# Kernel optimization log

Measured on AMD Instinct MI355X. Metric: run time of the kernel, lower is better.

Reference implementation:

```python
import jax, jax.numpy as jnp
import numpy as np
from jax import lax

DIM = 180
NUM_HEADS = 6
WS = 16                     # window_size
OWS = 24                    # overlap_win_size = int(16 * 1.5)
PAD = (OWS - WS) // 2       # 4
EPS = 1e-5


def setup_inputs() -> dict:
    key = jax.random.key(0)
    ks = jax.random.split(key, 4)
    B, H, W, C = 1, 256, 256, DIM
    x = jax.random.normal(ks[0], (B, H * W, C), dtype=jnp.float32)
    s = 0.05  # keep logits in a sane range
    return {
        "x": x,
        "norm_w": jnp.ones((C,), jnp.float32),
        "norm_b": jnp.zeros((C,), jnp.float32),
        "q_w": jax.random.normal(ks[1], (C, C), jnp.float32) * s,
        "q_b": jnp.zeros((C,), jnp.float32),
        "kv_w": jax.random.normal(ks[2], (C, 2 * C), jnp.float32) * s,
        "kv_b": jnp.zeros((2 * C,), jnp.float32),
        "proj_w": jax.random.normal(ks[3], (C, C), jnp.float32) * s,
        "proj_b": jnp.zeros((C,), jnp.float32),
        "H": H,
        "W": W,
    }


def _ocab(x, norm_w, norm_b, q_w, q_b, kv_w, kv_b, proj_w, proj_b, H, W):
    B, N, C = x.shape
    nh, hd = NUM_HEADS, C // NUM_HEADS
    scale = hd ** (-0.5)
    nHw, nWw = H // WS, W // WS
    nW = nHw * nWw

    shortcut = x
    # LayerNorm
    mu = jnp.mean(x, axis=-1, keepdims=True)
    var = jnp.var(x, axis=-1, keepdims=True)
    xn = (x - mu) * lax.rsqrt(var + EPS) * norm_w + norm_b

    feat = xn.reshape(B, H, W, C)

    # --- query: non-overlapping window partition -> [B*nW, WS*WS, C]
    qw = feat.reshape(B, nHw, WS, nWw, WS, C).transpose(0, 1, 3, 2, 4, 5)
    qw = qw.reshape(B * nW, WS * WS, C)
    q = qw @ q_w + q_b

    # --- key/value: overlapping windows via unfold (kernel=OWS, stride=WS, pad=PAD)
    feat_chw = feat.transpose(0, 3, 1, 2)  # [B, C, H, W]
    patches = lax.conv_general_dilated_patches(
        feat_chw, filter_shape=(OWS, OWS), window_strides=(WS, WS),
        padding=((PAD, PAD), (PAD, PAD)))  # [B, C*OWS*OWS, nHw, nWw], channel-major
    kv_feat = patches.reshape(B, C, OWS * OWS, nW).transpose(0, 3, 2, 1)
    kv_feat = kv_feat.reshape(B * nW, OWS * OWS, C)
    kv = kv_feat @ kv_w + kv_b
    k, v = jnp.split(kv, 2, axis=-1)

    # --- multi-head attention: 256 queries vs 576 keys per window
    q = q.reshape(B * nW, WS * WS, nh, hd).transpose(0, 2, 1, 3)
    k = k.reshape(B * nW, OWS * OWS, nh, hd).transpose(0, 2, 1, 3)
    v = v.reshape(B * nW, OWS * OWS, nh, hd).transpose(0, 2, 1, 3)

    attn = jnp.einsum('whqd,whkd->whqk', q, k) * scale
    attn = jax.nn.softmax(attn, axis=-1)
    out = jnp.einsum('whqk,whkd->whqd', attn, v)
    out = out.transpose(0, 2, 1, 3).reshape(B * nW, WS * WS, C)
    out = out @ proj_w + proj_b

    # --- window reverse + residual
    out = out.reshape(B, nHw, nWw, WS, WS, C).transpose(0, 1, 3, 2, 4, 5)
    out = out.reshape(B, N, C)
    return shortcut + out


def reference(x, norm_w, norm_b, q_w, q_b, kv_w, kv_b, proj_w, proj_b, H, W):
    return _ocab(x, norm_w, norm_b, q_w, q_b, kv_w, kv_b, proj_w, proj_b, H, W)
```

## Files before the change

kernel.cpp:

```cpp
#include <hip/hip_runtime.h>
#include <math.h>

typedef __bf16 bf16x8 __attribute__((ext_vector_type(8)));
typedef float f32x4 __attribute__((ext_vector_type(4)));
typedef unsigned short ushort_t;

static __device__ __forceinline__ unsigned short f2bf(float f) {
  union { float f; unsigned int u; } c; c.f = f;
  unsigned int u = c.u;
  unsigned int r = u + 0x7FFFu + ((u >> 16) & 1u);
  return (unsigned short)(r >> 16);
}

#define CDIM 180
#define CPAD 192
#define NTOK 65536

#define SCL2E 0.26339361f

static __device__ __forceinline__ unsigned pk_bf(float a, float b) {
  union { float f; unsigned u; } ca, cb; ca.f = a; cb.f = b;
  return __builtin_amdgcn_perm(cb.u, ca.u, 0x07060302u);
}

__global__ __launch_bounds__(256) void prep_k(
    const float* __restrict__ q_w, const float* __restrict__ q_b,
    const float* __restrict__ kv_w, const float* __restrict__ kv_b,
    const float* __restrict__ p_w, const float* __restrict__ p_b,
    ushort_t* __restrict__ wqkvt, ushort_t* __restrict__ pwt,
    float* __restrict__ qkvb, float* __restrict__ pbp,
    ushort_t* __restrict__ k_bias_row, ushort_t* __restrict__ vt4_bias_grp)
{
  int i = blockIdx.x * 256 + threadIdx.x;
  if (i < 110592) {
    int n = i / 192, k = i % 192;
    float v = 0.f;
    if (k < CDIM) {
      if (n < 192) { int h = n >> 5, d = n & 31; if (d < 30) v = q_w[k * CDIM + h * 30 + d] * SCL2E; }
      else { int cn = n - 192; int part = cn >= 192; int c2 = cn - part * 192;
             int h = c2 >> 5, d = c2 & 31;
             if (d < 30) v = kv_w[k * 360 + part * 180 + h * 30 + d]; }
    }
    wqkvt[i] = f2bf(v);
    return;
  }
  i -= 110592;
  if (i < 36864) {
    int n = i / 192, r = i % 192, h = r >> 5, d = r & 31;
    float v = (d < 30 && n < CDIM) ? p_w[(h * 30 + d) * CDIM + n] : 0.f;
    pwt[i] = f2bf(v);
    return;
  }
  i -= 36864;
  if (i < 576) {
    float v = 0.f;
    if (i < 192) { int h = i >> 5, d = i & 31; if (d < 30) v = q_b[h * 30 + d] * SCL2E; }
    else { int cn = i - 192; int part = cn >= 192; int c2 = cn - part * 192;
           int h = c2 >> 5, d = c2 & 31;
           if (d < 30) v = kv_b[part * 180 + h * 30 + d];
           else if (part == 1 && d == 30) v = 1.0f; }
    qkvb[i] = v;
    return;
  }
  i -= 576;
  if (i < 192) { pbp[i] = (i < CDIM) ? p_b[i] : 0.f; return; }
  i -= 192;
  if (i < 192) {
    int h = i >> 5, d = i & 31;
    k_bias_row[i] = (d < 30) ? f2bf(kv_b[h * 30 + d]) : (ushort_t)0;
    return;
  }
  i -= 192;
  if (i < 768) {
    int d = i >> 2, h = d >> 5, dd = d & 31;
    float v = 0.f;
    if (dd < 30) v = kv_b[180 + h * 30 + dd];
    else if (dd == 30) v = 1.0f;
    vt4_bias_grp[i] = f2bf(v);
    return;
  }
}

__global__ __launch_bounds__(256) void ln_k(const float* __restrict__ x,
    const float* __restrict__ nw, const float* __restrict__ nb,
    ushort_t* __restrict__ xn)
{
  const int lane = threadIdx.x & 63, wave = threadIdx.x >> 6;
  const int row = blockIdx.x * 4 + wave;
  const float* xr = x + (size_t)row * CDIM;
  float f0 = xr[lane];
  float f1 = xr[lane + 64];
  float f2 = (lane < 52) ? xr[lane + 128] : 0.f;
  float sum = f0 + f1 + f2;
  float sq = f0 * f0 + f1 * f1 + f2 * f2;
  #pragma unroll
  for (int off = 1; off < 64; off <<= 1) {
    sum += __shfl_xor(sum, off, 64);
    sq  += __shfl_xor(sq, off, 64);
  }
  const float inv_n = 1.0f / 180.0f;
  float mean = sum * inv_n;
  float var = sq * inv_n - mean * mean;
  float rs = rsqrtf(var + 1e-5f);
  ushort_t* xo = xn + (size_t)row * CPAD;
  #pragma unroll
  for (int e = 0; e < 3; ++e) {
    int col = lane + e * 64;
    float v = 0.f;
    if (col < CDIM) v = (( (e==0)?f0 : (e==1)?f1 : f2 ) - mean) * rs * nw[col] + nb[col];
    xo[col] = f2bf(v);
  }
}

template<int MODE>
__global__ __launch_bounds__(256) void gemm_k(const ushort_t* __restrict__ A,
    const ushort_t* __restrict__ Wt, const float* __restrict__ bias,
    ushort_t* __restrict__ q_out, ushort_t* __restrict__ k_out,
    ushort_t* __restrict__ vt_out,
    float* __restrict__ outf, const float* __restrict__ resid)
{
  constexpr int NT = (MODE == 0) ? 9 : 3;
  __shared__ __align__(16) ushort_t aS[128 * 200];
  const int tid = threadIdx.x;
  const int lane = tid & 63, wave = tid >> 6;
  const int quad = lane >> 4, l16 = lane & 15;
  const int wm = wave & 1, wn = wave >> 1;
  const int bm = blockIdx.x;

  {
    const ushort_t* Ab = A + (size_t)bm * 128 * 192;
    #pragma unroll
    for (int it = 0; it < 12; ++it) {
      int f = it * 256 + tid;
      int row = f / 24, kq = f % 24;
      uint4 v = *reinterpret_cast<const uint4*>(Ab + row * 192 + kq * 8);
      *reinterpret_cast<uint4*>(&aS[row * 200 + kq * 8]) = v;
    }
  }
  __syncthreads();

  for (int nt0 = 0; nt0 < NT; ++nt0) {
    f32x4 acc[4][2] = {};
    #pragma unroll
    for (int ks = 0; ks < 6; ++ks) {
      bf16x8 af[4], bfr[2];
      #pragma unroll
      for (int nt = 0; nt < 2; ++nt) {
        int n = nt0 * 64 + wn * 32 + nt * 16 + l16;
        bfr[nt] = *reinterpret_cast<const bf16x8*>(Wt + (size_t)n * 192 + ks * 32 + quad * 8);
      }
      #pragma unroll
      for (int mt = 0; mt < 4; ++mt)
        af[mt] = *reinterpret_cast<const bf16x8*>(&aS[(wm * 64 + mt * 16 + l16) * 200 + ks * 32 + quad * 8]);
      #pragma unroll
      for (int mt = 0; mt < 4; ++mt)
        #pragma unroll
        for (int nt = 0; nt < 2; ++nt)
          acc[mt][nt] = __builtin_amdgcn_mfma_f32_16x16x32_bf16(af[mt], bfr[nt], acc[mt][nt], 0, 0, 0);
    }
    #pragma unroll
    for (int mt = 0; mt < 4; ++mt) {
      int row = bm * 128 + wm * 64 + mt * 16 + quad * 4;
      #pragma unroll
      for (int nt = 0; nt < 2; ++nt) {
        int ncol = nt0 * 64 + wn * 32 + nt * 16 + l16;
        float bv = bias[ncol];
        if (MODE == 0 && nt0 >= 6) {
          int d = ncol - 384;
          unsigned p0 = pk_bf(acc[mt][nt][0] + bv, acc[mt][nt][1] + bv);
          unsigned p1 = pk_bf(acc[mt][nt][2] + bv, acc[mt][nt][3] + bv);
          uint2 val; val.x = p0; val.y = p1;
          *reinterpret_cast<uint2*>(vt_out + (size_t)row * 192 + d * 4) = val;
        } else {
          #pragma unroll
          for (int r = 0; r < 4; ++r) {
            int rr = row + r;
            float v = acc[mt][nt][r] + bv;
            if (MODE == 0) {
              if (ncol < 192) q_out[(size_t)rr * CPAD + ncol] = f2bf(v);
              else k_out[(size_t)rr * CPAD + (ncol - 192)] = f2bf(v);
            } else {
              if (ncol < CDIM) outf[(size_t)rr * CDIM + ncol] = v + resid[(size_t)rr * CDIM + ncol];
            }
          }
        }
      }
    }
  }
}

__global__ __launch_bounds__(256, 4) void attn_k(const ushort_t* __restrict__ q_tok,
    const ushort_t* __restrict__ k_tok, const ushort_t* __restrict__ vt4,
    ushort_t* __restrict__ ao)
{
  const int w = blockIdx.x, h = blockIdx.y;
  const int tid = threadIdx.x;
  const int lane = tid & 63, wave = tid >> 6;
  const int quad = lane >> 4, l16 = lane & 15;
  const int wy = w >> 4, wx = w & 15;
  const int tok0 = wy * 16 * 256 + wx * 16;
  const int hc = h * 32;
  const int ybase = wy * 16 - 4, xbase = wx * 16 - 4;

  bf16x8 qf[4];
  #pragma unroll
  for (int qt = 0; qt < 4; ++qt) {
    int qi = wave * 64 + qt * 16 + l16;
    int token = tok0 + (qi >> 4) * 256 + (qi & 15);
    qf[qt] = *reinterpret_cast<const bf16x8*>(q_tok + (size_t)token * CPAD + hc + quad * 8);
  }

  const int key0 = ((l16 >> 2) << 3) + (l16 & 3);

  int kpy[3][2], ktx[3][2]; bool kxin[3][2];
  int vpy[3][2], vtx[3][2]; bool vxin[3][2];
  #pragma unroll
  for (int cm = 0; cm < 3; ++cm) {
    #pragma unroll
    for (int j = 0; j < 2; ++j) {
      int pk = 32 * cm + key0 + 4 * j;
      int py = pk / 24, px = pk - py * 24;
      kpy[cm][j] = py; ktx[cm][j] = xbase + px;
      kxin[cm][j] = (unsigned)(xbase + px) < 256u;
      int pv = 32 * cm + quad * 8 + 4 * j;
      int pyv = pv / 24, pxv = pv - pyv * 24;
      vpy[cm][j] = pyv; vtx[cm][j] = xbase + pxv;
      vxin[cm][j] = (unsigned)(xbase + pxv) < 256u;
    }
  }
  const int dOff0 = (hc + l16) * 4, dOff1 = (hc + 16 + l16) * 4;

  f32x4 o[4][2] = {};
  f32x4 zero = {0.f, 0.f, 0.f, 0.f};

  #pragma unroll
  for (int c = 0; c < 18; ++c) {
    const int cm = c % 3, c3 = c / 3;
    const int yrow = ybase + 4 * c3;
    bf16x8 kf[2];
    #pragma unroll
    for (int kt = 0; kt < 2; ++kt) {
      int y = yrow + kpy[cm][kt];
      bool inb = kxin[cm][kt] && ((unsigned)y < 256u);
      int t = inb ? (y * 256 + ktx[cm][kt]) : NTOK;
      kf[kt] = *reinterpret_cast<const bf16x8*>(k_tok + (size_t)t * CPAD + hc + quad * 8);
    }
    unsigned vv[2][4];
    #pragma unroll
    for (int h2 = 0; h2 < 2; ++h2) {
      int y = yrow + vpy[cm][h2];
      bool inb = vxin[cm][h2] && ((unsigned)y < 256u);
      int t = inb ? (y * 256 + vtx[cm][h2]) : NTOK;
      const ushort_t* gp = vt4 + (size_t)t * 192;
      uint2 v0 = *reinterpret_cast<const uint2*>(gp + dOff0);
      uint2 v1 = *reinterpret_cast<const uint2*>(gp + dOff1);
      vv[0][h2 * 2] = v0.x; vv[0][h2 * 2 + 1] = v0.y;
      vv[1][h2 * 2] = v1.x; vv[1][h2 * 2 + 1] = v1.y;
    }
    bf16x8 vf[2];
    #pragma unroll
    for (int dt = 0; dt < 2; ++dt) {
      union { unsigned u[4]; bf16x8 v; } a_;
      a_.u[0] = vv[dt][0]; a_.u[1] = vv[dt][1];
      a_.u[2] = vv[dt][2]; a_.u[3] = vv[dt][3];
      vf[dt] = a_.v;
    }
    #pragma unroll
    for (int qt = 0; qt < 4; ++qt) {
      f32x4 s0 = __builtin_amdgcn_mfma_f32_16x16x32_bf16(kf[0], qf[qt], zero, 0, 0, 0);
      f32x4 s1 = __builtin_amdgcn_mfma_f32_16x16x32_bf16(kf[1], qf[qt], zero, 0, 0, 0);
      union { unsigned u[4]; bf16x8 v; } pk;
      pk.u[0] = pk_bf(__builtin_amdgcn_exp2f(s0[0]), __builtin_amdgcn_exp2f(s0[1]));
      pk.u[1] = pk_bf(__builtin_amdgcn_exp2f(s0[2]), __builtin_amdgcn_exp2f(s0[3]));
      pk.u[2] = pk_bf(__builtin_amdgcn_exp2f(s1[0]), __builtin_amdgcn_exp2f(s1[1]));
      pk.u[3] = pk_bf(__builtin_amdgcn_exp2f(s1[2]), __builtin_amdgcn_exp2f(s1[3]));
      #pragma unroll
      for (int dt = 0; dt < 2; ++dt)
        o[qt][dt] = __builtin_amdgcn_mfma_f32_16x16x32_bf16(pk.v, vf[dt], o[qt][dt], 0, 0, 0);
    }
  }

  #pragma unroll
  for (int qt = 0; qt < 4; ++qt) {
    #pragma unroll
    for (int r = 0; r < 4; ++r) {
      float l = __shfl(o[qt][1][r], (lane & 48) + 14, 64);
      float inv = 1.0f / l;
      int qi = wave * 64 + qt * 16 + quad * 4 + r;
      int token = tok0 + (qi >> 4) * 256 + (qi & 15);
      ao[(size_t)token * CPAD + hc + l16]      = f2bf(o[qt][0][r] * inv);
      ao[(size_t)token * CPAD + hc + 16 + l16] = f2bf(o[qt][1][r] * inv);
    }
  }
}

extern "C" void kernel_launch(void* const* d_in, const int* in_sizes, int n_in,
                              void* d_out, int out_size, void* d_ws, size_t ws_size,
                              hipStream_t stream) {
  const float* x      = (const float*)d_in[0];
  const float* norm_w = (const float*)d_in[1];
  const float* norm_b = (const float*)d_in[2];
  const float* q_w    = (const float*)d_in[3];
  const float* q_b    = (const float*)d_in[4];
  const float* kv_w   = (const float*)d_in[5];
  const float* kv_b   = (const float*)d_in[6];
  const float* p_w    = (const float*)d_in[7];
  const float* p_b    = (const float*)d_in[8];

  char* base = (char*)d_ws;
  size_t off = 0;
  auto alloc = [&](size_t bytes) { char* p = base + off; off = (off + bytes + 255) & ~(size_t)255; return p; };
  ushort_t* xn_p  = (ushort_t*)alloc((size_t)NTOK * CPAD * 2);
  ushort_t* q_tok = (ushort_t*)alloc((size_t)NTOK * CPAD * 2);
  ushort_t* k_tok = (ushort_t*)alloc((size_t)(NTOK + 1) * CPAD * 2);
  ushort_t* vt4   = (ushort_t*)alloc((size_t)(NTOK + 4) * 192 * 2);
  ushort_t* wqkvt = (ushort_t*)alloc(576 * 192 * 2);
  ushort_t* pwt   = (ushort_t*)alloc(192 * 192 * 2);
  float* qkvb = (float*)alloc(576 * 4);
  float* pbp  = (float*)alloc(192 * 4);
  ushort_t* ao = xn_p;

  prep_k<<<583, 256, 0, stream>>>(q_w, q_b, kv_w, kv_b, p_w, p_b,
                                  wqkvt, pwt, qkvb, pbp,
                                  k_tok + (size_t)NTOK * CPAD,
                                  vt4 + (size_t)NTOK * 192);
  ln_k<<<NTOK / 4, 256, 0, stream>>>(x, norm_w, norm_b, xn_p);
  gemm_k<0><<<NTOK / 128, 256, 0, stream>>>(xn_p, wqkvt, qkvb, q_tok, k_tok, vt4, nullptr, nullptr);
  attn_k<<<dim3(256, 6), 256, 0, stream>>>(q_tok, k_tok, vt4, ao);
  gemm_k<1><<<NTOK / 128, 256, 0, stream>>>(ao, pwt, pbp, nullptr, nullptr, nullptr, (float*)d_out, x);
}
```

Baseline: 239.3 us.

## Fuse LayerNorm into QKV GEMM and software-pipeline attention K/V loads

Removes the standalone LayerNorm kernel and computes the normalized bf16 rows straight into the QKV GEMM's shared-memory A tile. This avoids writing and re-reading the normalized activation buffer. The attention kernel now prefetches the next chunk's K and V fragments while the current MFMAs run, raises wave priority around the MFMA block, and bumps the occupancy hint to 5. The prefetch adds register pressure, which may conflict with the higher occupancy target and cause spills.

After: 300.9 us. 1.26x slower.

```diff
diff --git a/kernel.cpp b/kernel.cpp
--- a/kernel.cpp
+++ b/kernel.cpp
@@ -81,39 +81,9 @@
   }
 }
 
-__global__ __launch_bounds__(256) void ln_k(const float* __restrict__ x,
-    const float* __restrict__ nw, const float* __restrict__ nb,
-    ushort_t* __restrict__ xn)
-{
-  const int lane = threadIdx.x & 63, wave = threadIdx.x >> 6;
-  const int row = blockIdx.x * 4 + wave;
-  const float* xr = x + (size_t)row * CDIM;
-  float f0 = xr[lane];
-  float f1 = xr[lane + 64];
-  float f2 = (lane < 52) ? xr[lane + 128] : 0.f;
-  float sum = f0 + f1 + f2;
-  float sq = f0 * f0 + f1 * f1 + f2 * f2;
-  #pragma unroll
-  for (int off = 1; off < 64; off <<= 1) {
-    sum += __shfl_xor(sum, off, 64);
-    sq  += __shfl_xor(sq, off, 64);
-  }
-  const float inv_n = 1.0f / 180.0f;
-  float mean = sum * inv_n;
-  float var = sq * inv_n - mean * mean;
-  float rs = rsqrtf(var + 1e-5f);
-  ushort_t* xo = xn + (size_t)row * CPAD;
-  #pragma unroll
-  for (int e = 0; e < 3; ++e) {
-    int col = lane + e * 64;
-    float v = 0.f;
-    if (col < CDIM) v = (( (e==0)?f0 : (e==1)?f1 : f2 ) - mean) * rs * nw[col] + nb[col];
-    xo[col] = f2bf(v);
-  }
-}
-
 template<int MODE>
 __global__ __launch_bounds__(256) void gemm_k(const ushort_t* __restrict__ A,
+    const float* __restrict__ x, const float* __restrict__ nw, const float* __restrict__ nb,
     const ushort_t* __restrict__ Wt, const float* __restrict__ bias,
     ushort_t* __restrict__ q_out, ushort_t* __restrict__ k_out,
     ushort_t* __restrict__ vt_out,
@@ -127,7 +97,36 @@
   const int wm = wave & 1, wn = wave >> 1;
   const int bm = blockIdx.x;
 
-  {
+  if constexpr (MODE == 0) {
+    const float* xb = x + (size_t)bm * 128 * CDIM;
+    float w0 = nw[lane], b0 = nb[lane];
+    float w1 = nw[lane + 64], b1 = nb[lane + 64];
+    float w2 = (lane < 52) ? nw[lane + 128] : 0.f;
+    float b2 = (lane < 52) ? nb[lane + 128] : 0.f;
+    #pragma unroll 4
+    for (int r0 = 0; r0 < 32; ++r0) {
+      int row = wave * 32 + r0;
+      const float* xr = xb + (size_t)row * CDIM;
+      float f0 = xr[lane];
+      float f1 = xr[lane + 64];
+      float f2 = (lane < 52) ? xr[lane + 128] : 0.f;
+      float sum = f0 + f1 + f2;
+      float sq = f0 * f0 + f1 * f1 + f2 * f2;
+      #pragma unroll
+      for (int off = 1; off < 64; off <<= 1) {
+        sum += __shfl_xor(sum, off, 64);
+        sq  += __shfl_xor(sq, off, 64);
+      }
+      const float inv_n = 1.0f / 180.0f;
+      float mean = sum * inv_n;
+      float var = sq * inv_n - mean * mean;
+      float rs = rsqrtf(var + 1e-5f);
+      ushort_t* dst = &aS[row * 200];
+      dst[lane]       = f2bf((f0 - mean) * rs * w0 + b0);
+      dst[lane + 64]  = f2bf((f1 - mean) * rs * w1 + b1);
+      dst[lane + 128] = f2bf((lane < 52) ? ((f2 - mean) * rs * w2 + b2) : 0.f);
+    }
+  } else {
     const ushort_t* Ab = A + (size_t)bm * 128 * 192;
     #pragma unroll
     for (int it = 0; it < 12; ++it) {
@@ -189,7 +188,7 @@
   }
 }
 
-__global__ __launch_bounds__(256, 4) void attn_k(const ushort_t* __restrict__ q_tok,
+__global__ __launch_bounds__(256, 5) void attn_k(const ushort_t* __restrict__ q_tok,
     const ushort_t* __restrict__ k_tok, const ushort_t* __restrict__ vt4,
     ushort_t* __restrict__ ao)
 {
@@ -230,14 +229,9 @@
   }
   const int dOff0 = (hc + l16) * 4, dOff1 = (hc + 16 + l16) * 4;
 
-  f32x4 o[4][2] = {};
-  f32x4 zero = {0.f, 0.f, 0.f, 0.f};
-
-  #pragma unroll
-  for (int c = 0; c < 18; ++c) {
+  auto loadK = [&](int c, bf16x8* kf) {
     const int cm = c % 3, c3 = c / 3;
     const int yrow = ybase + 4 * c3;
-    bf16x8 kf[2];
     #pragma unroll
     for (int kt = 0; kt < 2; ++kt) {
       int y = yrow + kpy[cm][kt];
@@ -245,26 +239,43 @@
       int t = inb ? (y * 256 + ktx[cm][kt]) : NTOK;
       kf[kt] = *reinterpret_cast<const bf16x8*>(k_tok + (size_t)t * CPAD + hc + quad * 8);
     }
-    unsigned vv[2][4];
+  };
+  auto loadV = [&](int c, uint2* va, uint2* vb) {
+    const int cm = c % 3, c3 = c / 3;
+    const int yrow = ybase + 4 * c3;
     #pragma unroll
     for (int h2 = 0; h2 < 2; ++h2) {
       int y = yrow + vpy[cm][h2];
       bool inb = vxin[cm][h2] && ((unsigned)y < 256u);
       int t = inb ? (y * 256 + vtx[cm][h2]) : NTOK;
       const ushort_t* gp = vt4 + (size_t)t * 192;
-      uint2 v0 = *reinterpret_cast<const uint2*>(gp + dOff0);
-      uint2 v1 = *reinterpret_cast<const uint2*>(gp + dOff1);
-      vv[0][h2 * 2] = v0.x; vv[0][h2 * 2 + 1] = v0.y;
-      vv[1][h2 * 2] = v1.x; vv[1][h2 * 2 + 1] = v1.y;
-    }
+      va[h2] = *reinterpret_cast<const uint2*>(gp + dOff0);
+      vb[h2] = *reinterpret_cast<const uint2*>(gp + dOff1);
+    }
+  };
+
+  f32x4 o[4][2] = {};
+  f32x4 zero = {0.f, 0.f, 0.f, 0.f};
+
+  bf16x8 kf[2]; uint2 va[2], vb[2];
+  loadK(0, kf);
+  loadV(0, va, vb);
+
+  #pragma unroll
+  for (int c = 0; c < 18; ++c) {
+    bf16x8 kfn[2]; uint2 van[2], vbn[2];
+    if (c < 17) { loadK(c + 1, kfn); loadV(c + 1, van, vbn); }
+
     bf16x8 vf[2];
-    #pragma unroll
-    for (int dt = 0; dt < 2; ++dt) {
+    {
       union { unsigned u[4]; bf16x8 v; } a_;
-      a_.u[0] = vv[dt][0]; a_.u[1] = vv[dt][1];
-      a_.u[2] = vv[dt][2]; a_.u[3] = vv[dt][3];
-      vf[dt] = a_.v;
-    }
+      a_.u[0] = va[0].x; a_.u[1] = va[0].y; a_.u[2] = va[1].x; a_.u[3] = va[1].y;
+      vf[0] = a_.v;
+      a_.u[0] = vb[0].x; a_.u[1] = vb[0].y; a_.u[2] = vb[1].x; a_.u[3] = vb[1].y;
+      vf[1] = a_.v;
+    }
+
+    __builtin_amdgcn_s_setprio(1);
     #pragma unroll
     for (int qt = 0; qt < 4; ++qt) {
       f32x4 s0 = __builtin_amdgcn_mfma_f32_16x16x32_bf16(kf[0], qf[qt], zero, 0, 0, 0);
@@ -277,6 +288,12 @@
       #pragma unroll
       for (int dt = 0; dt < 2; ++dt)
         o[qt][dt] = __builtin_amdgcn_mfma_f32_16x16x32_bf16(pk.v, vf[dt], o[qt][dt], 0, 0, 0);
+    }
+    __builtin_amdgcn_s_setprio(0);
+
+    if (c < 17) {
+      #pragma unroll
+      for (int i = 0; i < 2; ++i) { kf[i] = kfn[i]; va[i] = van[i]; vb[i] = vbn[i]; }
     }
   }
 
@@ -310,7 +327,7 @@
   char* base = (char*)d_ws;
   size_t off = 0;
   auto alloc = [&](size_t bytes) { char* p = base + off; off = (off + bytes + 255) & ~(size_t)255; return p; };
-  ushort_t* xn_p  = (ushort_t*)alloc((size_t)NTOK * CPAD * 2);
+  ushort_t* ao    = (ushort_t*)alloc((size_t)NTOK * CPAD * 2);
   ushort_t* q_tok = (ushort_t*)alloc((size_t)NTOK * CPAD * 2);
   ushort_t* k_tok = (ushort_t*)alloc((size_t)(NTOK + 1) * CPAD * 2);
   ushort_t* vt4   = (ushort_t*)alloc((size_t)(NTOK + 4) * 192 * 2);
@@ -318,14 +335,14 @@
   ushort_t* pwt   = (ushort_t*)alloc(192 * 192 * 2);
   float* qkvb = (float*)alloc(576 * 4);
   float* pbp  = (float*)alloc(192 * 4);
-  ushort_t* ao = xn_p;
 
   prep_k<<<583, 256, 0, stream>>>(q_w, q_b, kv_w, kv_b, p_w, p_b,
                                   wqkvt, pwt, qkvb, pbp,
                                   k_tok + (size_t)NTOK * CPAD,
                                   vt4 + (size_t)NTOK * 192);
-  ln_k<<<NTOK / 4, 256, 0, stream>>>(x, norm_w, norm_b, xn_p);
-  gemm_k<0><<<NTOK / 128, 256, 0, stream>>>(xn_p, wqkvt, qkvb, q_tok, k_tok, vt4, nullptr, nullptr);
+  gemm_k<0><<<NTOK / 128, 256, 0, stream>>>(nullptr, x, norm_w, norm_b,
+                                            wqkvt, qkvb, q_tok, k_tok, vt4, nullptr, nullptr);
   attn_k<<<dim3(256, 6), 256, 0, stream>>>(q_tok, k_tok, vt4, ao);
-  gemm_k<1><<<NTOK / 128, 256, 0, stream>>>(ao, pwt, pbp, nullptr, nullptr, nullptr, (float*)d_out, x);
-}
+  gemm_k<1><<<NTOK / 128, 256, 0, stream>>>(ao, nullptr, nullptr, nullptr,
+                                            pwt, pbp, nullptr, nullptr, nullptr, (float*)d_out, x);
+}
```
